# Performance work log

Hardware: AMD Instinct MI355X
Metric: run time of the kernel (lower is better)

## Reference

```python
import jax, jax.numpy as jnp
import numpy as np

N, NF, DIM, H, DH, DEPTH, EDIM, NB = 256, 127, 128, 8, 64, 6, 3, 512
INNER = H * DH  # 512
SCALE = DH ** -0.5
EPS = 1e-5


def setup_inputs() -> dict:
    key = jax.random.key(0)
    ks = jax.random.split(key, 16)
    p = lambda k, shape: jax.random.normal(k, shape, jnp.float32) * 0.02
    return {
        "coordinates": jax.random.normal(ks[0], (N, 3), jnp.float32),
        "bonds": jax.random.randint(ks[1], (NB, 2), 0, N),
        "noise_level": jax.random.uniform(ks[2], (1,), jnp.float32),
        "atom_emb": p(ks[3], (N, NF)),
        "ln1_g": jnp.ones((DEPTH, DIM)), "ln1_b": jnp.zeros((DEPTH, DIM)),
        "Wq": p(ks[4], (DEPTH, DIM, INNER)), "bq": jnp.zeros((DEPTH, INNER)),
        "Wkv": p(ks[5], (DEPTH, DIM, 2 * INNER)), "bkv": jnp.zeros((DEPTH, 2 * INNER)),
        "We": p(ks[6], (DEPTH, EDIM, INNER)), "be": jnp.zeros((DEPTH, INNER)),
        "Wo": p(ks[7], (DEPTH, INNER, DIM)), "bo": jnp.zeros((DEPTH, DIM)),
        "Wg1": p(ks[8], (DEPTH, 3 * DIM)),
        "ln2_g": jnp.ones((DEPTH, DIM)), "ln2_b": jnp.zeros((DEPTH, DIM)),
        "W1": p(ks[9], (DEPTH, DIM, 4 * DIM)), "b1": jnp.zeros((DEPTH, 4 * DIM)),
        "W2": p(ks[10], (DEPTH, 4 * DIM, DIM)), "b2": jnp.zeros((DEPTH, DIM)),
        "Wg2": p(ks[11], (DEPTH, 3 * DIM)),
        "out_w": p(ks[12], (DIM, 1)), "out_b": jnp.zeros((1,)),
    }


def _layernorm(x, g, b):
    m = jnp.mean(x, axis=-1, keepdims=True)
    v = jnp.mean((x - m) ** 2, axis=-1, keepdims=True)
    return (x - m) * jax.lax.rsqrt(v + EPS) * g + b


def _gated_residual(x, res, Wg):
    # Linear(3*dim -> 1, no bias) then sigmoid; mask is all-True so no masking.
    gate = jax.nn.sigmoid(jnp.concatenate([x, res, x - res], axis=-1) @ Wg)[..., None]
    return x * gate + res * (1.0 - gate)


def _forward(coordinates, bonds, noise_level, atom_emb, ln1_g, ln1_b, Wq, bq,
             Wkv, bkv, We, be, Wo, bo, Wg1, ln2_g, ln2_b, W1, b1, W2, b2, Wg2,
             out_w, out_b):
    n = coordinates.shape[0]
    # nodes: [n, NF] atom embeddings (looked up at arange(n)) + noise column -> [n, DIM]
    noise_col = jnp.broadcast_to(noise_level.reshape(1, 1), (n, 1))
    nodes = jnp.concatenate([atom_emb, noise_col], axis=-1)
    # dense edge tensor [n, n, 3]: coordinate differences at bonded pairs, antisymmetric
    bi, bj = bonds[:, 0], bonds[:, 1]
    diff = coordinates[bi] - coordinates[bj]
    edges = jnp.zeros((n, n, EDIM), jnp.float32).at[bi, bj].set(diff).at[bj, bi].set(-diff)

    for l in range(DEPTH):
        # --- edge-biased multi-head attention (PreNorm) ---
        x = _layernorm(nodes, ln1_g[l], ln1_b[l])
        q = (x @ Wq[l] + bq[l]).reshape(n, H, DH).transpose(1, 0, 2)          # [h, i, d]
        kv = x @ Wkv[l] + bkv[l]
        k = kv[:, :INNER].reshape(n, H, DH).transpose(1, 0, 2)                # [h, j, d]
        v = kv[:, INNER:].reshape(n, H, DH).transpose(1, 0, 2)                # [h, j, d]
        e = (edges @ We[l] + be[l]).reshape(n, n, H, DH).transpose(2, 0, 1, 3)  # [h, i, j, d]
        k_ij = k[:, None, :, :] + e                                            # [h, i, j, d]
        v_ij = v[:, None, :, :] + e
        sim = jnp.einsum('hid,hijd->hij', q, k_ij) * SCALE
        attn = jax.nn.softmax(sim, axis=-1)  # mask is all ones -> no-op
        out = jnp.einsum('hij,hijd->hid', attn, v_ij)                          # [h, i, d]
        out = out.transpose(1, 0, 2).reshape(n, INNER) @ Wo[l] + bo[l]         # [n, DIM]
        nodes = _gated_residual(out, nodes, Wg1[l])
        # --- feedforward (PreNorm) + gated residual ---
        y = _layernorm(nodes, ln2_g[l], ln2_b[l])
        y = jax.nn.gelu(y @ W1[l] + b1[l], approximate=False) @ W2[l] + b2[l]
        nodes = _gated_residual(y, nodes, Wg2[l])

    energy = nodes @ out_w + out_b  # [n, 1]
    return energy[None, :, :]       # [1, n, 1]


def reference(coordinates, bonds, noise_level, atom_emb, ln1_g, ln1_b, Wq, bq,
              Wkv, bkv, We, be, Wo, bo, Wg1, ln2_g, ln2_b, W1, b1, W2, b2, Wg2,
              out_w, out_b):
    return _forward(coordinates, bonds, noise_level, atom_emb, ln1_g, ln1_b,
                    Wq, bq, Wkv, bkv, We, be, Wo, bo, Wg1, ln2_g, ln2_b,
                    W1, b1, W2, b2, Wg2, out_w, out_b)
```

## Files before the change

### kernel.cpp

```cpp
#include <hip/hip_runtime.h>

#define NN     256
#define NF     127
#define DIM    128
#define NH     8
#define DH     64
#define INNER  512
#define DEPTH  6
#define NB     512
#define ATTN_SCALE 0.125f
#define LN_EPS 1e-5f

__device__ __forceinline__ float wred_sum(float v){
#pragma unroll
  for(int o=32;o;o>>=1) v += __shfl_xor(v,o);
  return v;
}
__device__ __forceinline__ float wred_max(float v){
#pragma unroll
  for(int o=32;o;o>>=1) v = fmaxf(v,__shfl_xor(v,o));
  return v;
}
__device__ __forceinline__ float block_sum(float v, float* sred, int t){
  v = wred_sum(v);
  __syncthreads();
  if((t&63)==0) sred[t>>6]=v;
  __syncthreads();
  float s = 0.f;
#pragma unroll
  for(int w=0; w<8; w++) s += sred[w];
  return s;
}

__device__ __forceinline__ void dev_ln(const float* in, float* out,
                                       const float* g, const float* b,
                                       float* sred, int t){
  float v = (t<DIM)? in[t] : 0.f;
  float m = block_sum(v,sred,t) * (1.f/DIM);
  float d = (t<DIM)? (v-m) : 0.f;
  float var = block_sum(d*d,sred,t) * (1.f/DIM);
  float rs = rsqrtf(var + LN_EPS);
  if(t<DIM) out[t] = d*rs*g[t] + b[t];
  __syncthreads();
}

__device__ __forceinline__ void dev_qkv4(const float* xs, int i,
    const float* Wq, const float* bq, const float* Wkv, const float* bkv,
    const float* be, float* qg, float* kT, float* vg, float* redS, int t){
  {
    const int cg4 = (t&127)*4, rq = t>>7;
    float4 acc = make_float4(0.f,0.f,0.f,0.f);
#pragma unroll
    for(int f=rq*32; f<rq*32+32; f++){
      float x = xs[f];
      float4 w = *(const float4*)(Wq + f*INNER + cg4);
      acc.x=fmaf(x,w.x,acc.x); acc.y=fmaf(x,w.y,acc.y);
      acc.z=fmaf(x,w.z,acc.z); acc.w=fmaf(x,w.w,acc.w);
    }
    *(float4*)(redS + rq*INNER + cg4) = acc;
  }
  __syncthreads();
  qg[i*INNER+t] = bq[t] + redS[t] + redS[INNER+t] + redS[2*INNER+t] + redS[3*INNER+t];
  __syncthreads();
  {
    const int cg4 = (t&255)*4, rh = t>>8;
    float4 acc = make_float4(0.f,0.f,0.f,0.f);
#pragma unroll 8
    for(int f=rh*64; f<rh*64+64; f++){
      float x = xs[f];
      float4 w = *(const float4*)(Wkv + f*(2*INNER) + cg4);
      acc.x=fmaf(x,w.x,acc.x); acc.y=fmaf(x,w.y,acc.y);
      acc.z=fmaf(x,w.z,acc.z); acc.w=fmaf(x,w.w,acc.w);
    }
    *(float4*)(redS + rh*(2*INNER) + cg4) = acc;
  }
  __syncthreads();
#pragma unroll
  for(int cc=0; cc<2; cc++){
    int c = t + cc*512;
    float s = redS[c] + redS[2*INNER+c] + bkv[c];
    if(c < INNER) kT[c*NN+i]          = s + be[c];
    else          vg[i*INNER+c-INNER] = s + be[c-INNER];
  }
  __syncthreads();
}

__global__ __launch_bounds__(512) void k_qkv0(const float* atom_emb, const float* noise,
    float* nodes,
    const float* ln1_g, const float* ln1_b,
    const float* Wq, const float* bq, const float* Wkv, const float* bkv, const float* be,
    float* qg, float* kT, float* vg){
  __shared__ float nd[DIM], xs[DIM], sred[8], redS[2048];
  int t = threadIdx.x, i = blockIdx.x;
  if(t<DIM){
    float v = (t<NF)? atom_emb[i*NF+t] : noise[0];
    nd[t] = v;
    nodes[i*DIM+t] = v;
  }
  __syncthreads();
  dev_ln(nd, xs, ln1_g, ln1_b, sred, t);
  dev_qkv4(xs, i, Wq, bq, Wkv, bkv, be, qg, kT, vg, redS, t);
}

__global__ __launch_bounds__(512) void k_layer(
    float* nodes, const float* qg, const float* kT, const float* vg,
    float* qg_n, float* kT_n, float* vg_n,
    const int* bonds, const float* coords,
    const float* We,
    const float* Wo, const float* bo, const float* Wg1,
    const float* ln2_g, const float* ln2_b,
    const float* W1, const float* b1, const float* W2, const float* b2,
    const float* Wg2,
    const float* ln1_g_n, const float* ln1_b_n,
    const float* Wq_n, const float* bq_n, const float* Wkv_n, const float* bkv_n,
    const float* be_n, int has_next)
{
  __shared__ float nd[DIM], xs[DIM], qs[INNER], ao[INNER], o128[DIM];
  __shared__ float eL[NN*3], aW[NH*NN], redS[2048], sred[8], qWe[NH*3];
  const int t = threadIdx.x, i = blockIdx.x;

  if(t<DIM) nd[t] = nodes[i*DIM+t];
  qs[t] = qg[i*INNER+t];
  eL[t] = 0.f;
  if(t<NN) eL[512+t] = 0.f;
  __syncthreads();

  {
    int bi = bonds[2*t], bj = bonds[2*t+1];
    if(bi==i || bj==i){
      float dx = coords[3*bi+0] - coords[3*bj+0];
      float dy = coords[3*bi+1] - coords[3*bj+1];
      float dz = coords[3*bi+2] - coords[3*bj+2];
      if(bi==i){ eL[bj*3+0]=dx;  eL[bj*3+1]=dy;  eL[bj*3+2]=dz;  }
      if(bj==i){ eL[bi*3+0]=-dx; eL[bi*3+1]=-dy; eL[bi*3+2]=-dz; }
    }
  }
  __syncthreads();

  if(t < NH*3){
    int h = t/3, c = t%3;
    float acc = 0.f;
    for(int d=0; d<DH; d++) acc = fmaf(qs[h*DH+d], We[c*INNER + h*DH + d], acc);
    qWe[t] = acc;
  }
  __syncthreads();

  {
    const int h = t>>6, l = t&63, j0 = 4*l;
    const float* kTh = kT + (h*DH)*NN;
    float s0=0.f,s1=0.f,s2=0.f,s3=0.f;
#pragma unroll 8
    for(int o=0; o<DH; o++){
      float qv = qs[h*DH+o];
      float4 kk = *(const float4*)(kTh + o*NN + j0);
      s0=fmaf(qv,kk.x,s0); s1=fmaf(qv,kk.y,s1); s2=fmaf(qv,kk.z,s2); s3=fmaf(qv,kk.w,s3);
    }
    float w0=qWe[h*3+0], w1=qWe[h*3+1], w2=qWe[h*3+2];
    s0 += w0*eL[(j0+0)*3+0] + w1*eL[(j0+0)*3+1] + w2*eL[(j0+0)*3+2];
    s1 += w0*eL[(j0+1)*3+0] + w1*eL[(j0+1)*3+1] + w2*eL[(j0+1)*3+2];
    s2 += w0*eL[(j0+2)*3+0] + w1*eL[(j0+2)*3+1] + w2*eL[(j0+2)*3+2];
    s3 += w0*eL[(j0+3)*3+0] + w1*eL[(j0+3)*3+1] + w2*eL[(j0+3)*3+2];
    s0*=ATTN_SCALE; s1*=ATTN_SCALE; s2*=ATTN_SCALE; s3*=ATTN_SCALE;
    float mx = wred_max(fmaxf(fmaxf(s0,s1),fmaxf(s2,s3)));
    float p0=expf(s0-mx), p1=expf(s1-mx), p2=expf(s2-mx), p3=expf(s3-mx);
    float inv = 1.f / wred_sum(p0+p1+p2+p3);
    float a0=p0*inv, a1=p1*inv, a2=p2*inv, a3=p3*inv;
    float* aw = aW + h*NN;
    *(float4*)(aw + j0) = make_float4(a0,a1,a2,a3);
    float c0 = a0*eL[(j0+0)*3+0]+a1*eL[(j0+1)*3+0]+a2*eL[(j0+2)*3+0]+a3*eL[(j0+3)*3+0];
    float c1 = a0*eL[(j0+0)*3+1]+a1*eL[(j0+1)*3+1]+a2*eL[(j0+2)*3+1]+a3*eL[(j0+3)*3+1];
    float c2 = a0*eL[(j0+0)*3+2]+a1*eL[(j0+1)*3+2]+a2*eL[(j0+2)*3+2]+a3*eL[(j0+3)*3+2];
    c0 = wred_sum(c0); c1 = wred_sum(c1); c2 = wred_sum(c2);
    __builtin_amdgcn_wave_barrier();
    const int dq = (l&15)*4, jg = l>>4;
    const float* vb = vg + h*DH + dq;
    float4 acc = make_float4(0.f,0.f,0.f,0.f);
#pragma unroll 8
    for(int jj=0; jj<64; jj++){
      int j = jg*64 + jj;
      float a = aw[j];
      float4 vv = *(const float4*)(vb + j*INNER);
      acc.x=fmaf(a,vv.x,acc.x); acc.y=fmaf(a,vv.y,acc.y);
      acc.z=fmaf(a,vv.z,acc.z); acc.w=fmaf(a,vv.w,acc.w);
    }
#pragma unroll
    for(int o=16;o<64;o<<=1){
      acc.x += __shfl_xor(acc.x,o); acc.y += __shfl_xor(acc.y,o);
      acc.z += __shfl_xor(acc.z,o); acc.w += __shfl_xor(acc.w,o);
    }
    if(l<16){
      float4 we0 = *(const float4*)(We + 0*INNER + h*DH + dq);
      float4 we1 = *(const float4*)(We + 1*INNER + h*DH + dq);
      float4 we2 = *(const float4*)(We + 2*INNER + h*DH + dq);
      float4 o;
      o.x = acc.x + c0*we0.x + c1*we1.x + c2*we2.x;
      o.y = acc.y + c0*we0.y + c1*we1.y + c2*we2.y;
      o.z = acc.z + c0*we0.z + c1*we1.z + c2*we2.z;
      o.w = acc.w + c0*we0.w + c1*we1.w + c2*we2.w;
      *(float4*)(ao + h*DH + dq) = o;
    }
  }
  __syncthreads();

  {
    const int cg4 = (t&31)*4, rg = t>>5;
    float4 acc = make_float4(0.f,0.f,0.f,0.f);
#pragma unroll
    for(int r=rg*32; r<rg*32+32; r++){
      float a = ao[r];
      float4 w = *(const float4*)(Wo + r*DIM + cg4);
      acc.x=fmaf(a,w.x,acc.x); acc.y=fmaf(a,w.y,acc.y);
      acc.z=fmaf(a,w.z,acc.z); acc.w=fmaf(a,w.w,acc.w);
    }
    *(float4*)(redS + rg*DIM + cg4) = acc;
    __syncthreads();
    if(t<DIM){
      float s = bo[t];
#pragma unroll
      for(int g=0; g<16; g++) s += redS[g*DIM+t];
      o128[t] = s;
    }
    __syncthreads();
    float gv = 0.f;
    if(t<DIM){
      float o = o128[t], r = nd[t];
      gv = o*Wg1[t] + r*Wg1[DIM+t] + (o-r)*Wg1[2*DIM+t];
    }
    float gs = block_sum(gv, sred, t);
    float gate = 1.f/(1.f + expf(-gs));
    if(t<DIM) nd[t] = o128[t]*gate + nd[t]*(1.f-gate);
    __syncthreads();
  }

  dev_ln(nd, xs, ln2_g, ln2_b, sred, t);
  {
    const int cg4 = (t&127)*4, rq = t>>7;
    float4 acc = make_float4(0.f,0.f,0.f,0.f);
#pragma unroll
    for(int f=rq*32; f<rq*32+32; f++){
      float x = xs[f];
      float4 w = *(const float4*)(W1 + f*INNER + cg4);
      acc.x=fmaf(x,w.x,acc.x); acc.y=fmaf(x,w.y,acc.y);
      acc.z=fmaf(x,w.z,acc.z); acc.w=fmaf(x,w.w,acc.w);
    }
    *(float4*)(redS + rq*INNER + cg4) = acc;
  }
  __syncthreads();
  {
    float a = b1[t] + redS[t] + redS[INNER+t] + redS[2*INNER+t] + redS[3*INNER+t];
    qs[t] = 0.5f*a*(1.f + erff(a*0.70710678118654752440f));
  }
  __syncthreads();
  {
    const int cg4 = (t&31)*4, rg = t>>5;
    float4 acc = make_float4(0.f,0.f,0.f,0.f);
#pragma unroll
    for(int m=rg*32; m<rg*32+32; m++){
      float a = qs[m];
      float4 w = *(const float4*)(W2 + m*DIM + cg4);
      acc.x=fmaf(a,w.x,acc.x); acc.y=fmaf(a,w.y,acc.y);
      acc.z=fmaf(a,w.z,acc.z); acc.w=fmaf(a,w.w,acc.w);
    }
    *(float4*)(redS + rg*DIM + cg4) = acc;
    __syncthreads();
    if(t<DIM){
      float s = b2[t];
#pragma unroll
      for(int g=0; g<16; g++) s += redS[g*DIM+t];
      o128[t] = s;
    }
    __syncthreads();
    float gv = 0.f;
    if(t<DIM){
      float y = o128[t], r = nd[t];
      gv = y*Wg2[t] + r*Wg2[DIM+t] + (y-r)*Wg2[2*DIM+t];
    }
    float gs = block_sum(gv, sred, t);
    float gate = 1.f/(1.f + expf(-gs));
    if(t<DIM) nd[t] = o128[t]*gate + nd[t]*(1.f-gate);
    __syncthreads();
  }
  if(t<DIM) nodes[i*DIM+t] = nd[t];

  if(has_next){
    dev_ln(nd, xs, ln1_g_n, ln1_b_n, sred, t);
    dev_qkv4(xs, i, Wq_n, bq_n, Wkv_n, bkv_n, be_n, qg_n, kT_n, vg_n, redS, t);
  }
}

__global__ __launch_bounds__(64) void k_energy(const float* nodes, const float* out_w,
                                               const float* out_b, float* out){
  int i = blockIdx.x, l = threadIdx.x;
  float a = fmaf(nodes[i*DIM+l], out_w[l], nodes[i*DIM+64+l]*out_w[64+l]);
  a = wred_sum(a);
  if(l==0) out[i] = a + out_b[0];
}

extern "C" void kernel_launch(void* const* d_in, const int* in_sizes, int n_in,
                              void* d_out, int out_size, void* d_ws, size_t ws_size,
                              hipStream_t stream){
  const float* coords   = (const float*)d_in[0];
  const int*   bonds    = (const int*  )d_in[1];
  const float* noise    = (const float*)d_in[2];
  const float* atom_emb = (const float*)d_in[3];
  const float* ln1_g = (const float*)d_in[4];
  const float* ln1_b = (const float*)d_in[5];
  const float* Wq    = (const float*)d_in[6];
  const float* bq    = (const float*)d_in[7];
  const float* Wkv   = (const float*)d_in[8];
  const float* bkv   = (const float*)d_in[9];
  const float* We    = (const float*)d_in[10];
  const float* be    = (const float*)d_in[11];
  const float* Wo    = (const float*)d_in[12];
  const float* bo    = (const float*)d_in[13];
  const float* Wg1   = (const float*)d_in[14];
  const float* ln2_g = (const float*)d_in[15];
  const float* ln2_b = (const float*)d_in[16];
  const float* W1    = (const float*)d_in[17];
  const float* b1    = (const float*)d_in[18];
  const float* W2    = (const float*)d_in[19];
  const float* b2    = (const float*)d_in[20];
  const float* Wg2   = (const float*)d_in[21];
  const float* out_w = (const float*)d_in[22];
  const float* out_b = (const float*)d_in[23];

  float* ws = (float*)d_ws;
  float* nodes   = ws;
  float* qbuf[2] = { ws +  32768, ws + 163840 };
  float* kbuf[2] = { ws + 294912, ws + 425984 };
  float* vbuf[2] = { ws + 557056, ws + 688128 };

  k_qkv0<<<256, 512, 0, stream>>>(atom_emb, noise, nodes, ln1_g, ln1_b,
                                  Wq, bq, Wkv, bkv, be,
                                  qbuf[0], kbuf[0], vbuf[0]);
  for(int l=0; l<DEPTH; l++){
    int cur = l&1, nxt = cur^1;
    int has_next = (l < DEPTH-1);
    int ln = has_next ? l+1 : l;
    k_layer<<<256, 512, 0, stream>>>(
      nodes, qbuf[cur], kbuf[cur], vbuf[cur],
      qbuf[nxt], kbuf[nxt], vbuf[nxt],
      bonds, coords,
      We  + (size_t)l*3*INNER,
      Wo  + (size_t)l*INNER*DIM, bo + (size_t)l*DIM, Wg1 + (size_t)l*3*DIM,
      ln2_g + (size_t)l*DIM, ln2_b + (size_t)l*DIM,
      W1  + (size_t)l*DIM*4*DIM, b1 + (size_t)l*4*DIM,
      W2  + (size_t)l*4*DIM*DIM, b2 + (size_t)l*DIM, Wg2 + (size_t)l*3*DIM,
      ln1_g + (size_t)ln*DIM, ln1_b + (size_t)ln*DIM,
      Wq  + (size_t)ln*DIM*INNER, bq + (size_t)ln*INNER,
      Wkv + (size_t)ln*DIM*2*INNER, bkv + (size_t)ln*2*INNER,
      be  + (size_t)ln*INNER, has_next);
  }
  k_energy<<<256, 64, 0, stream>>>(nodes, out_w, out_b, (float*)d_out);
}
```

Measured before the change: 320.2 us.

## Process four atoms per block to reuse weight and K/V loads

Each block now handles four node rows instead of one, so every weight, K and V element loaded from global memory feeds four rows of FMAs. Grid size drops from 256 to 64 blocks. The final energy projection is folded into the last layer kernel, which removes a separate launch. The cost is fewer blocks than compute units on the GPU, plus more registers and shared memory per block, which lowers parallelism and occupancy.

After: 510.9 us. 59.5% more time.

```diff
diff --git a/kernel.cpp b/kernel.cpp
--- a/kernel.cpp
+++ b/kernel.cpp
@@ -8,98 +8,153 @@
 #define INNER  512
 #define DEPTH  6
 #define NB     512
+#define R      4
 #define ATTN_SCALE 0.125f
 #define LN_EPS 1e-5f
 
+#define FMA4(A_, S_, V_) { A_.x=fmaf(S_,(V_).x,A_.x); A_.y=fmaf(S_,(V_).y,A_.y); \
+                           A_.z=fmaf(S_,(V_).z,A_.z); A_.w=fmaf(S_,(V_).w,A_.w); }
+
 __device__ __forceinline__ float wred_sum(float v){
 #pragma unroll
   for(int o=32;o;o>>=1) v += __shfl_xor(v,o);
   return v;
 }
-__device__ __forceinline__ float wred_max(float v){
-#pragma unroll
-  for(int o=32;o;o>>=1) v = fmaxf(v,__shfl_xor(v,o));
-  return v;
-}
-__device__ __forceinline__ float block_sum(float v, float* sred, int t){
+
+__device__ __forceinline__ float row_sum128(float v, float* sred, int t){
   v = wred_sum(v);
   __syncthreads();
-  if((t&63)==0) sred[t>>6]=v;
-  __syncthreads();
-  float s = 0.f;
-#pragma unroll
-  for(int w=0; w<8; w++) s += sred[w];
-  return s;
-}
-
-__device__ __forceinline__ void dev_ln(const float* in, float* out,
-                                       const float* g, const float* b,
-                                       float* sred, int t){
-  float v = (t<DIM)? in[t] : 0.f;
-  float m = block_sum(v,sred,t) * (1.f/DIM);
-  float d = (t<DIM)? (v-m) : 0.f;
-  float var = block_sum(d*d,sred,t) * (1.f/DIM);
-  float rs = rsqrtf(var + LN_EPS);
-  if(t<DIM) out[t] = d*rs*g[t] + b[t];
-  __syncthreads();
-}
-
-__device__ __forceinline__ void dev_qkv4(const float* xs, int i,
+  if((t&63)==0) sred[t>>6] = v;
+  __syncthreads();
+  const int r2 = (t>>7)<<1;
+  return sred[r2] + sred[r2+1];
+}
+
+__device__ __forceinline__ void dev_ln4(const float* in, float* out,
+                                        const float* g, const float* b,
+                                        float* sred, int t){
+  const int d = t&127;
+  float v = in[t];
+  float m = row_sum128(v, sred, t) * (1.f/DIM);
+  float dv = v - m;
+  float var = row_sum128(dv*dv, sred, t) * (1.f/DIM);
+  out[t] = dv * rsqrtf(var + LN_EPS) * g[d] + b[d];
+  __syncthreads();
+}
+
+__device__ __forceinline__ void dev_gate(const float* o, float* nd, const float* Wg,
+                                         float* sred, int t){
+  const int d = t&127;
+  float ov = o[t], rv = nd[t];
+  float gv = ov*Wg[d] + rv*Wg[DIM+d] + (ov-rv)*Wg[2*DIM+d];
+  float gate = 1.f/(1.f + expf(-row_sum128(gv, sred, t)));
+  nd[t] = ov*gate + rv*(1.f-gate);
+  __syncthreads();
+}
+
+__device__ __forceinline__ void mm128_512_part(const float* xin, const float* W,
+                                               float* SC, int t){
+  const int cg4 = (t&127)<<2, fq = t>>7;
+  float4 a0=make_float4(0.f,0.f,0.f,0.f), a1=a0, a2=a0, a3=a0;
+#pragma unroll 8
+  for(int f=fq*32; f<fq*32+32; f++){
+    float4 wv = *(const float4*)(W + f*INNER + cg4);
+    float v0=xin[f], v1=xin[DIM+f], v2=xin[2*DIM+f], v3=xin[3*DIM+f];
+    FMA4(a0,v0,wv); FMA4(a1,v1,wv); FMA4(a2,v2,wv); FMA4(a3,v3,wv);
+  }
+  float* p = SC + (fq*R)*INNER + cg4;
+  *(float4*)(p)           = a0;
+  *(float4*)(p +   INNER) = a1;
+  *(float4*)(p + 2*INNER) = a2;
+  *(float4*)(p + 3*INNER) = a3;
+}
+
+__device__ __forceinline__ void mm128_1024_part(const float* xin, const float* W,
+                                                float* SC, int t){
+  const int cg4 = (t&255)<<2, fh = t>>8;
+  float4 a0=make_float4(0.f,0.f,0.f,0.f), a1=a0, a2=a0, a3=a0;
+#pragma unroll 8
+  for(int f=fh*64; f<fh*64+64; f++){
+    float4 wv = *(const float4*)(W + f*(2*INNER) + cg4);
+    float v0=xin[f], v1=xin[DIM+f], v2=xin[2*DIM+f], v3=xin[3*DIM+f];
+    FMA4(a0,v0,wv); FMA4(a1,v1,wv); FMA4(a2,v2,wv); FMA4(a3,v3,wv);
+  }
+  float* p = SC + (fh*R)*(2*INNER) + cg4;
+  *(float4*)(p)             = a0;
+  *(float4*)(p +   2*INNER) = a1;
+  *(float4*)(p + 2*2*INNER) = a2;
+  *(float4*)(p + 3*2*INNER) = a3;
+}
+
+__device__ __forceinline__ void mm512_128_part(const float* ain, const float* W,
+                                               float* SC, int t){
+  const int cg4 = (t&31)<<2, fg = t>>5;
+  float4 a0=make_float4(0.f,0.f,0.f,0.f), a1=a0, a2=a0, a3=a0;
+#pragma unroll 8
+  for(int f=fg*32; f<fg*32+32; f++){
+    float4 wv = *(const float4*)(W + f*DIM + cg4);
+    float v0=ain[f], v1=ain[INNER+f], v2=ain[2*INNER+f], v3=ain[3*INNER+f];
+    FMA4(a0,v0,wv); FMA4(a1,v1,wv); FMA4(a2,v2,wv); FMA4(a3,v3,wv);
+  }
+  float* p = SC + (fg*R)*DIM + cg4;
+  *(float4*)(p)         = a0;
+  *(float4*)(p +   DIM) = a1;
+  *(float4*)(p + 2*DIM) = a2;
+  *(float4*)(p + 3*DIM) = a3;
+}
+
+__device__ __forceinline__ void red512_128(const float* SC, const float* bias,
+                                           float* o128, int t){
+  const int r = t>>7, d = t&127;
+  float s = bias[d];
+#pragma unroll
+  for(int fg=0; fg<16; fg++) s += SC[(fg*R + r)*DIM + d];
+  o128[t] = s;
+}
+
+__device__ __forceinline__ void dev_qkv(const float* xs, int i0,
     const float* Wq, const float* bq, const float* Wkv, const float* bkv,
-    const float* be, float* qg, float* kT, float* vg, float* redS, int t){
-  {
-    const int cg4 = (t&127)*4, rq = t>>7;
-    float4 acc = make_float4(0.f,0.f,0.f,0.f);
-#pragma unroll
-    for(int f=rq*32; f<rq*32+32; f++){
-      float x = xs[f];
-      float4 w = *(const float4*)(Wq + f*INNER + cg4);
-      acc.x=fmaf(x,w.x,acc.x); acc.y=fmaf(x,w.y,acc.y);
-      acc.z=fmaf(x,w.z,acc.z); acc.w=fmaf(x,w.w,acc.w);
-    }
-    *(float4*)(redS + rq*INNER + cg4) = acc;
-  }
-  __syncthreads();
-  qg[i*INNER+t] = bq[t] + redS[t] + redS[INNER+t] + redS[2*INNER+t] + redS[3*INNER+t];
-  __syncthreads();
-  {
-    const int cg4 = (t&255)*4, rh = t>>8;
-    float4 acc = make_float4(0.f,0.f,0.f,0.f);
-#pragma unroll 8
-    for(int f=rh*64; f<rh*64+64; f++){
-      float x = xs[f];
-      float4 w = *(const float4*)(Wkv + f*(2*INNER) + cg4);
-      acc.x=fmaf(x,w.x,acc.x); acc.y=fmaf(x,w.y,acc.y);
-      acc.z=fmaf(x,w.z,acc.z); acc.w=fmaf(x,w.w,acc.w);
-    }
-    *(float4*)(redS + rh*(2*INNER) + cg4) = acc;
-  }
-  __syncthreads();
-#pragma unroll
-  for(int cc=0; cc<2; cc++){
-    int c = t + cc*512;
-    float s = redS[c] + redS[2*INNER+c] + bkv[c];
-    if(c < INNER) kT[c*NN+i]          = s + be[c];
-    else          vg[i*INNER+c-INNER] = s + be[c-INNER];
+    const float* be, float* qg, float* kT, float* vg, float* SC, int t){
+  mm128_512_part(xs, Wq, SC, t);
+  __syncthreads();
+#pragma unroll
+  for(int cc=0; cc<4; cc++){
+    int idx = cc*512 + t;
+    int r = idx>>9, c = idx&511;
+    float s = bq[c] + SC[r*INNER+c] + SC[(R+r)*INNER+c]
+                    + SC[(2*R+r)*INNER+c] + SC[(3*R+r)*INNER+c];
+    qg[(i0+r)*INNER + c] = s;
+  }
+  __syncthreads();
+  mm128_1024_part(xs, Wkv, SC, t);
+  __syncthreads();
+#pragma unroll
+  for(int cc=0; cc<8; cc++){
+    int idx = cc*512 + t;
+    int r = idx>>10, c = idx&1023;
+    float s = bkv[c] + SC[r*(2*INNER)+c] + SC[(R+r)*(2*INNER)+c];
+    if(c < INNER) kT[c*NN + i0 + r]            = s + be[c];
+    else          vg[(i0+r)*INNER + (c-INNER)] = s + be[c-INNER];
   }
   __syncthreads();
 }
 
 __global__ __launch_bounds__(512) void k_qkv0(const float* atom_emb, const float* noise,
-    float* nodes,
-    const float* ln1_g, const float* ln1_b,
+    float* nodes, const float* ln1_g, const float* ln1_b,
     const float* Wq, const float* bq, const float* Wkv, const float* bkv, const float* be,
     float* qg, float* kT, float* vg){
-  __shared__ float nd[DIM], xs[DIM], sred[8], redS[2048];
-  int t = threadIdx.x, i = blockIdx.x;
-  if(t<DIM){
-    float v = (t<NF)? atom_emb[i*NF+t] : noise[0];
+  __shared__ __align__(16) float SC[8192];
+  __shared__ float nd[R*DIM], xsm[R*DIM], sred[8];
+  const int t = threadIdx.x, i0 = blockIdx.x*R;
+  {
+    const int r = t>>7, d = t&127;
+    float v = (d<NF)? atom_emb[(i0+r)*NF + d] : noise[0];
     nd[t] = v;
-    nodes[i*DIM+t] = v;
-  }
-  __syncthreads();
-  dev_ln(nd, xs, ln1_g, ln1_b, sred, t);
-  dev_qkv4(xs, i, Wq, bq, Wkv, bkv, be, qg, kT, vg, redS, t);
+    nodes[i0*DIM + t] = v;
+  }
+  __syncthreads();
+  dev_ln4(nd, xsm, ln1_g, ln1_b, sred, t);
+  dev_qkv(xsm, i0, Wq, bq, Wkv, bkv, be, qg, kT, vg, SC, t);
 }
 
 __global__ __launch_bounds__(512) void k_layer(
@@ -113,187 +168,213 @@
     const float* Wg2,
     const float* ln1_g_n, const float* ln1_b_n,
     const float* Wq_n, const float* bq_n, const float* Wkv_n, const float* bkv_n,
-    const float* be_n, int has_next)
+    const float* be_n,
+    const float* out_w, const float* out_b, float* eout, int has_next)
 {
-  __shared__ float nd[DIM], xs[DIM], qs[INNER], ao[INNER], o128[DIM];
-  __shared__ float eL[NN*3], aW[NH*NN], redS[2048], sred[8], qWe[NH*3];
-  const int t = threadIdx.x, i = blockIdx.x;
-
-  if(t<DIM) nd[t] = nodes[i*DIM+t];
-  qs[t] = qg[i*INNER+t];
-  eL[t] = 0.f;
-  if(t<NN) eL[512+t] = 0.f;
+  __shared__ __align__(16) float SC[8192];
+  __shared__ __align__(16) float qs[R*INNER];
+  __shared__ __align__(16) float eb[3*R*NN];
+  __shared__ __align__(16) float ao[R*INNER];
+  __shared__ float nd[R*DIM], xsm[R*DIM];
+  float* o128 = eb;
+  float* sred = eb + R*DIM;
+  const int t = threadIdx.x, i0 = blockIdx.x*R;
+
+  nd[t] = nodes[i0*DIM + t];
+#pragma unroll
+  for(int cc=0; cc<4; cc++) qs[cc*512 + t] = qg[i0*INNER + cc*512 + t];
+#pragma unroll
+  for(int cc=0; cc<6; cc++) eb[cc*512 + t] = 0.f;
   __syncthreads();
 
   {
-    int bi = bonds[2*t], bj = bonds[2*t+1];
-    if(bi==i || bj==i){
+    const int bi = bonds[2*t], bj = bonds[2*t+1];
+    const bool hi = (bi>=i0 && bi<i0+R), hj = (bj>=i0 && bj<i0+R);
+    if(hi || hj){
       float dx = coords[3*bi+0] - coords[3*bj+0];
       float dy = coords[3*bi+1] - coords[3*bj+1];
       float dz = coords[3*bi+2] - coords[3*bj+2];
-      if(bi==i){ eL[bj*3+0]=dx;  eL[bj*3+1]=dy;  eL[bj*3+2]=dz;  }
-      if(bj==i){ eL[bi*3+0]=-dx; eL[bi*3+1]=-dy; eL[bi*3+2]=-dz; }
-    }
-  }
-  __syncthreads();
-
-  if(t < NH*3){
-    int h = t/3, c = t%3;
-    float acc = 0.f;
-    for(int d=0; d<DH; d++) acc = fmaf(qs[h*DH+d], We[c*INNER + h*DH + d], acc);
-    qWe[t] = acc;
+      if(hi){ int r = bi-i0;
+        eb[r*NN+bj]=dx;  eb[(R+r)*NN+bj]=dy;  eb[(2*R+r)*NN+bj]=dz;  }
+      if(hj){ int r = bj-i0;
+        eb[r*NN+bi]=-dx; eb[(R+r)*NN+bi]=-dy; eb[(2*R+r)*NN+bi]=-dz; }
+    }
   }
   __syncthreads();
 
   {
-    const int h = t>>6, l = t&63, j0 = 4*l;
-    const float* kTh = kT + (h*DH)*NN;
-    float s0=0.f,s1=0.f,s2=0.f,s3=0.f;
+    const int h = t>>6, l = t&63, j0 = l<<2;
+    const int qb = h*DH;
+    float qwe[R][3];
+    {
+      float qv0=qs[0*INNER+qb+l], qv1=qs[1*INNER+qb+l],
+            qv2=qs[2*INNER+qb+l], qv3=qs[3*INNER+qb+l];
+#pragma unroll
+      for(int c=0;c<3;c++){
+        float wv = We[c*INNER + qb + l];
+        qwe[0][c]=qv0*wv; qwe[1][c]=qv1*wv; qwe[2][c]=qv2*wv; qwe[3][c]=qv3*wv;
+      }
+#pragma unroll
+      for(int o=32;o;o>>=1)
+#pragma unroll
+        for(int r=0;r<R;r++){
+          qwe[r][0]+=__shfl_xor(qwe[r][0],o);
+          qwe[r][1]+=__shfl_xor(qwe[r][1],o);
+          qwe[r][2]+=__shfl_xor(qwe[r][2],o);
+        }
+    }
+    const float* kTh = kT + qb*NN;
+    float s[R][4];
+#pragma unroll
+    for(int r=0;r<R;r++){ s[r][0]=0.f; s[r][1]=0.f; s[r][2]=0.f; s[r][3]=0.f; }
 #pragma unroll 8
-    for(int o=0; o<DH; o++){
-      float qv = qs[h*DH+o];
+    for(int o=0;o<DH;o++){
       float4 kk = *(const float4*)(kTh + o*NN + j0);
-      s0=fmaf(qv,kk.x,s0); s1=fmaf(qv,kk.y,s1); s2=fmaf(qv,kk.z,s2); s3=fmaf(qv,kk.w,s3);
-    }
-    float w0=qWe[h*3+0], w1=qWe[h*3+1], w2=qWe[h*3+2];
-    s0 += w0*eL[(j0+0)*3+0] + w1*eL[(j0+0)*3+1] + w2*eL[(j0+0)*3+2];
-    s1 += w0*eL[(j0+1)*3+0] + w1*eL[(j0+1)*3+1] + w2*eL[(j0+1)*3+2];
-    s2 += w0*eL[(j0+2)*3+0] + w1*eL[(j0+2)*3+1] + w2*eL[(j0+2)*3+2];
-    s3 += w0*eL[(j0+3)*3+0] + w1*eL[(j0+3)*3+1] + w2*eL[(j0+3)*3+2];
-    s0*=ATTN_SCALE; s1*=ATTN_SCALE; s2*=ATTN_SCALE; s3*=ATTN_SCALE;
-    float mx = wred_max(fmaxf(fmaxf(s0,s1),fmaxf(s2,s3)));
-    float p0=expf(s0-mx), p1=expf(s1-mx), p2=expf(s2-mx), p3=expf(s3-mx);
-    float inv = 1.f / wred_sum(p0+p1+p2+p3);
-    float a0=p0*inv, a1=p1*inv, a2=p2*inv, a3=p3*inv;
-    float* aw = aW + h*NN;
-    *(float4*)(aw + j0) = make_float4(a0,a1,a2,a3);
-    float c0 = a0*eL[(j0+0)*3+0]+a1*eL[(j0+1)*3+0]+a2*eL[(j0+2)*3+0]+a3*eL[(j0+3)*3+0];
-    float c1 = a0*eL[(j0+0)*3+1]+a1*eL[(j0+1)*3+1]+a2*eL[(j0+2)*3+1]+a3*eL[(j0+3)*3+1];
-    float c2 = a0*eL[(j0+0)*3+2]+a1*eL[(j0+1)*3+2]+a2*eL[(j0+2)*3+2]+a3*eL[(j0+3)*3+2];
-    c0 = wred_sum(c0); c1 = wred_sum(c1); c2 = wred_sum(c2);
+#pragma unroll
+      for(int r=0;r<R;r++){
+        float qv = qs[r*INNER + qb + o];
+        s[r][0]=fmaf(qv,kk.x,s[r][0]); s[r][1]=fmaf(qv,kk.y,s[r][1]);
+        s[r][2]=fmaf(qv,kk.z,s[r][2]); s[r][3]=fmaf(qv,kk.w,s[r][3]);
+      }
+    }
+#pragma unroll
+    for(int r=0;r<R;r++){
+      float4 ex = *(const float4*)(eb + r*NN + j0);
+      float4 ey = *(const float4*)(eb + (R+r)*NN + j0);
+      float4 ez = *(const float4*)(eb + (2*R+r)*NN + j0);
+      float w0=qwe[r][0], w1=qwe[r][1], w2=qwe[r][2];
+      s[r][0] = (s[r][0] + w0*ex.x + w1*ey.x + w2*ez.x)*ATTN_SCALE;
+      s[r][1] = (s[r][1] + w0*ex.y + w1*ey.y + w2*ez.y)*ATTN_SCALE;
+      s[r][2] = (s[r][2] + w0*ex.z + w1*ey.z + w2*ez.z)*ATTN_SCALE;
+      s[r][3] = (s[r][3] + w0*ex.w + w1*ey.w + w2*ez.w)*ATTN_SCALE;
+    }
+    float mx[R];
+#pragma unroll
+    for(int r=0;r<R;r++) mx[r]=fmaxf(fmaxf(s[r][0],s[r][1]),fmaxf(s[r][2],s[r][3]));
+#pragma unroll
+    for(int o=32;o;o>>=1)
+#pragma unroll
+      for(int r=0;r<R;r++) mx[r]=fmaxf(mx[r],__shfl_xor(mx[r],o));
+    float sm[R];
+#pragma unroll
+    for(int r=0;r<R;r++){
+      s[r][0]=expf(s[r][0]-mx[r]); s[r][1]=expf(s[r][1]-mx[r]);
+      s[r][2]=expf(s[r][2]-mx[r]); s[r][3]=expf(s[r][3]-mx[r]);
+      sm[r]=s[r][0]+s[r][1]+s[r][2]+s[r][3];
+    }
+#pragma unroll
+    for(int o=32;o;o>>=1)
+#pragma unroll
+      for(int r=0;r<R;r++) sm[r]+=__shfl_xor(sm[r],o);
+    float cE[R][3];
+#pragma unroll
+    for(int r=0;r<R;r++){
+      float inv = 1.f/sm[r];
+      float a0=s[r][0]*inv, a1=s[r][1]*inv, a2=s[r][2]*inv, a3=s[r][3]*inv;
+      *(float4*)(SC + ((r<<3)+h)*NN + j0) = make_float4(a0,a1,a2,a3);
+      float4 ex = *(const float4*)(eb + r*NN + j0);
+      float4 ey = *(const float4*)(eb + (R+r)*NN + j0);
+      float4 ez = *(const float4*)(eb + (2*R+r)*NN + j0);
+      cE[r][0]=a0*ex.x+a1*ex.y+a2*ex.z+a3*ex.w;
+      cE[r][1]=a0*ey.x+a1*ey.y+a2*ey.z+a3*ey.w;
+      cE[r][2]=a0*ez.x+a1*ez.y+a2*ez.z+a3*ez.w;
+    }
+#pragma unroll
+    for(int o=32;o;o>>=1)
+#pragma unroll
+      for(int r=0;r<R;r++){
+        cE[r][0]+=__shfl_xor(cE[r][0],o);
+        cE[r][1]+=__shfl_xor(cE[r][1],o);
+        cE[r][2]+=__shfl_xor(cE[r][2],o);
+      }
     __builtin_amdgcn_wave_barrier();
-    const int dq = (l&15)*4, jg = l>>4;
-    const float* vb = vg + h*DH + dq;
-    float4 acc = make_float4(0.f,0.f,0.f,0.f);
+    const int dq=(l&15)<<2, jg=l>>4;
+    const float* vb = vg + qb + dq;
+    float4 acc0=make_float4(0.f,0.f,0.f,0.f), acc1=acc0, acc2=acc0, acc3=acc0;
 #pragma unroll 8
-    for(int jj=0; jj<64; jj++){
-      int j = jg*64 + jj;
-      float a = aw[j];
+    for(int jj=0;jj<64;jj++){
+      int j = (jg<<6) + ((jj + (jg<<3)) & 63);
       float4 vv = *(const float4*)(vb + j*INNER);
-      acc.x=fmaf(a,vv.x,acc.x); acc.y=fmaf(a,vv.y,acc.y);
-      acc.z=fmaf(a,vv.z,acc.z); acc.w=fmaf(a,vv.w,acc.w);
+      float w0 = SC[(0*NH+h)*NN + j];
+      float w1 = SC[(1*NH+h)*NN + j];
+      float w2 = SC[(2*NH+h)*NN + j];
+      float w3 = SC[(3*NH+h)*NN + j];
+      FMA4(acc0,w0,vv); FMA4(acc1,w1,vv); FMA4(acc2,w2,vv); FMA4(acc3,w3,vv);
     }
 #pragma unroll
     for(int o=16;o<64;o<<=1){
-      acc.x += __shfl_xor(acc.x,o); acc.y += __shfl_xor(acc.y,o);
-      acc.z += __shfl_xor(acc.z,o); acc.w += __shfl_xor(acc.w,o);
+      acc0.x+=__shfl_xor(acc0.x,o); acc0.y+=__shfl_xor(acc0.y,o);
+      acc0.z+=__shfl_xor(acc0.z,o); acc0.w+=__shfl_xor(acc0.w,o);
+      acc1.x+=__shfl_xor(acc1.x,o); acc1.y+=__shfl_xor(acc1.y,o);
+      acc1.z+=__shfl_xor(acc1.z,o); acc1.w+=__shfl_xor(acc1.w,o);
+      acc2.x+=__shfl_xor(acc2.x,o); acc2.y+=__shfl_xor(acc2.y,o);
+      acc2.z+=__shfl_xor(acc2.z,o); acc2.w+=__shfl_xor(acc2.w,o);
+      acc3.x+=__shfl_xor(acc3.x,o); acc3.y+=__shfl_xor(acc3.y,o);
+      acc3.z+=__shfl_xor(acc3.z,o); acc3.w+=__shfl_xor(acc3.w,o);
     }
     if(l<16){
-      float4 we0 = *(const float4*)(We + 0*INNER + h*DH + dq);
-      float4 we1 = *(const float4*)(We + 1*INNER + h*DH + dq);
-      float4 we2 = *(const float4*)(We + 2*INNER + h*DH + dq);
-      float4 o;
-      o.x = acc.x + c0*we0.x + c1*we1.x + c2*we2.x;
-      o.y = acc.y + c0*we0.y + c1*we1.y + c2*we2.y;
-      o.z = acc.z + c0*we0.z + c1*we1.z + c2*we2.z;
-      o.w = acc.w + c0*we0.w + c1*we1.w + c2*we2.w;
-      *(float4*)(ao + h*DH + dq) = o;
-    }
-  }
-  __syncthreads();
-
-  {
-    const int cg4 = (t&31)*4, rg = t>>5;
-    float4 acc = make_float4(0.f,0.f,0.f,0.f);
-#pragma unroll
-    for(int r=rg*32; r<rg*32+32; r++){
-      float a = ao[r];
-      float4 w = *(const float4*)(Wo + r*DIM + cg4);
-      acc.x=fmaf(a,w.x,acc.x); acc.y=fmaf(a,w.y,acc.y);
-      acc.z=fmaf(a,w.z,acc.z); acc.w=fmaf(a,w.w,acc.w);
-    }
-    *(float4*)(redS + rg*DIM + cg4) = acc;
-    __syncthreads();
-    if(t<DIM){
-      float s = bo[t];
-#pragma unroll
-      for(int g=0; g<16; g++) s += redS[g*DIM+t];
-      o128[t] = s;
-    }
-    __syncthreads();
-    float gv = 0.f;
-    if(t<DIM){
-      float o = o128[t], r = nd[t];
-      gv = o*Wg1[t] + r*Wg1[DIM+t] + (o-r)*Wg1[2*DIM+t];
-    }
-    float gs = block_sum(gv, sred, t);
-    float gate = 1.f/(1.f + expf(-gs));
-    if(t<DIM) nd[t] = o128[t]*gate + nd[t]*(1.f-gate);
-    __syncthreads();
-  }
-
-  dev_ln(nd, xs, ln2_g, ln2_b, sred, t);
-  {
-    const int cg4 = (t&127)*4, rq = t>>7;
-    float4 acc = make_float4(0.f,0.f,0.f,0.f);
-#pragma unroll
-    for(int f=rq*32; f<rq*32+32; f++){
-      float x = xs[f];
-      float4 w = *(const float4*)(W1 + f*INNER + cg4);
-      acc.x=fmaf(x,w.x,acc.x); acc.y=fmaf(x,w.y,acc.y);
-      acc.z=fmaf(x,w.z,acc.z); acc.w=fmaf(x,w.w,acc.w);
-    }
-    *(float4*)(redS + rq*INNER + cg4) = acc;
-  }
-  __syncthreads();
-  {
-    float a = b1[t] + redS[t] + redS[INNER+t] + redS[2*INNER+t] + redS[3*INNER+t];
-    qs[t] = 0.5f*a*(1.f + erff(a*0.70710678118654752440f));
-  }
-  __syncthreads();
-  {
-    const int cg4 = (t&31)*4, rg = t>>5;
-    float4 acc = make_float4(0.f,0.f,0.f,0.f);
-#pragma unroll
-    for(int m=rg*32; m<rg*32+32; m++){
-      float a = qs[m];
-      float4 w = *(const float4*)(W2 + m*DIM + cg4);
-      acc.x=fmaf(a,w.x,acc.x); acc.y=fmaf(a,w.y,acc.y);
-      acc.z=fmaf(a,w.z,acc.z); acc.w=fmaf(a,w.w,acc.w);
-    }
-    *(float4*)(redS + rg*DIM + cg4) = acc;
-    __syncthreads();
-    if(t<DIM){
-      float s = b2[t];
-#pragma unroll
-      for(int g=0; g<16; g++) s += redS[g*DIM+t];
-      o128[t] = s;
-    }
-    __syncthreads();
-    float gv = 0.f;
-    if(t<DIM){
-      float y = o128[t], r = nd[t];
-      gv = y*Wg2[t] + r*Wg2[DIM+t] + (y-r)*Wg2[2*DIM+t];
-    }
-    float gs = block_sum(gv, sred, t);
-    float gate = 1.f/(1.f + expf(-gs));
-    if(t<DIM) nd[t] = o128[t]*gate + nd[t]*(1.f-gate);
-    __syncthreads();
-  }
-  if(t<DIM) nodes[i*DIM+t] = nd[t];
+      float4 we0 = *(const float4*)(We + 0*INNER + qb + dq);
+      float4 we1 = *(const float4*)(We + 1*INNER + qb + dq);
+      float4 we2 = *(const float4*)(We + 2*INNER + qb + dq);
+      float4 ov;
+      ov.x=acc0.x+cE[0][0]*we0.x+cE[0][1]*we1.x+cE[0][2]*we2.x;
+      ov.y=acc0.y+cE[0][0]*we0.y+cE[0][1]*we1.y+cE[0][2]*we2.y;
+      ov.z=acc0.z+cE[0][0]*we0.z+cE[0][1]*we1.z+cE[0][2]*we2.z;
+      ov.w=acc0.w+cE[0][0]*we0.w+cE[0][1]*we1.w+cE[0][2]*we2.w;
+      *(float4*)(ao + 0*INNER + qb + dq) = ov;
+      ov.x=acc1.x+cE[1][0]*we0.x+cE[1][1]*we1.x+cE[1][2]*we2.x;
+      ov.y=acc1.y+cE[1][0]*we0.y+cE[1][1]*we1.y+cE[1][2]*we2.y;
+      ov.z=acc1.z+cE[1][0]*we0.z+cE[1][1]*we1.z+cE[1][2]*we2.z;
+      ov.w=acc1.w+cE[1][0]*we0.w+cE[1][1]*we1.w+cE[1][2]*we2.w;
+      *(float4*)(ao + 1*INNER + qb + dq) = ov;
+      ov.x=acc2.x+cE[2][0]*we0.x+cE[2][1]*we1.x+cE[2][2]*we2.x;
+      ov.y=acc2.y+cE[2][0]*we0.y+cE[2][1]*we1.y+cE[2][2]*we2.y;
+      ov.z=acc2.z+cE[2][0]*we0.z+cE[2][1]*we1.z+cE[2][2]*we2.z;
+      ov.w=acc2.w+cE[2][0]*we0.w+cE[2][1]*we1.w+cE[2][2]*we2.w;
+      *(float4*)(ao + 2*INNER + qb + dq) = ov;
+      ov.x=acc3.x+cE[3][0]*we0.x+cE[3][1]*we1.x+cE[3][2]*we2.x;
+      ov.y=acc3.y+cE[3][0]*we0.y+cE[3][1]*we1.y+cE[3][2]*we2.y;
+      ov.z=acc3.z+cE[3][0]*we0.z+cE[3][1]*we1.z+cE[3][2]*we2.z;
+      ov.w=acc3.w+cE[3][0]*we0.w+cE[3][1]*we1.w+cE[3][2]*we2.w;
+      *(float4*)(ao + 3*INNER + qb + dq) = ov;
+    }
+  }
+  __syncthreads();
+
+  mm512_128_part(ao, Wo, SC, t);
+  __syncthreads();
+  red512_128(SC, bo, o128, t);
+  __syncthreads();
+  dev_gate(o128, nd, Wg1, sred, t);
+
+  dev_ln4(nd, xsm, ln2_g, ln2_b, sred, t);
+  mm128_512_part(xsm, W1, SC, t);
+  __syncthreads();
+#pragma unroll
+  for(int cc=0; cc<4; cc++){
+    int idx = cc*512 + t;
+    int r = idx>>9, c = idx&511;
+    float a = b1[c] + SC[r*INNER+c] + SC[(R+r)*INNER+c]
+                    + SC[(2*R+r)*INNER+c] + SC[(3*R+r)*INNER+c];
+    qs[idx] = 0.5f*a*(1.f + erff(a*0.70710678118654752440f));
+  }
+  __syncthreads();
+  mm512_128_part(qs, W2, SC, t);
+  __syncthreads();
+  red512_128(SC, b2, o128, t);
+  __syncthreads();
+  dev_gate(o128, nd, Wg2, sred, t);
+
+  nodes[i0*DIM + t] = nd[t];
 
   if(has_next){
-    dev_ln(nd, xs, ln1_g_n, ln1_b_n, sred, t);
-    dev_qkv4(xs, i, Wq_n, bq_n, Wkv_n, bkv_n, be_n, qg_n, kT_n, vg_n, redS, t);
-  }
-}
-
-__global__ __launch_bounds__(64) void k_energy(const float* nodes, const float* out_w,
-                                               const float* out_b, float* out){
-  int i = blockIdx.x, l = threadIdx.x;
-  float a = fmaf(nodes[i*DIM+l], out_w[l], nodes[i*DIM+64+l]*out_w[64+l]);
-  a = wred_sum(a);
-  if(l==0) out[i] = a + out_b[0];
+    dev_ln4(nd, xsm, ln1_g_n, ln1_b_n, sred, t);
+    dev_qkv(xsm, i0, Wq_n, bq_n, Wkv_n, bkv_n, be_n, qg_n, kT_n, vg_n, SC, t);
+  } else {
+    float ev = nd[t] * out_w[t&127];
+    float es = row_sum128(ev, sred, t);
+    if((t&127)==0) eout[i0 + (t>>7)] = es + out_b[0];
+  }
 }
 
 extern "C" void kernel_launch(void* const* d_in, const int* in_sizes, int n_in,
@@ -330,14 +411,14 @@
   float* kbuf[2] = { ws + 294912, ws + 425984 };
   float* vbuf[2] = { ws + 557056, ws + 688128 };
 
-  k_qkv0<<<256, 512, 0, stream>>>(atom_emb, noise, nodes, ln1_g, ln1_b,
-                                  Wq, bq, Wkv, bkv, be,
-                                  qbuf[0], kbuf[0], vbuf[0]);
+  k_qkv0<<<NN/R, 512, 0, stream>>>(atom_emb, noise, nodes, ln1_g, ln1_b,
+                                   Wq, bq, Wkv, bkv, be,
+                                   qbuf[0], kbuf[0], vbuf[0]);
   for(int l=0; l<DEPTH; l++){
     int cur = l&1, nxt = cur^1;
     int has_next = (l < DEPTH-1);
     int ln = has_next ? l+1 : l;
-    k_layer<<<256, 512, 0, stream>>>(
+    k_layer<<<NN/R, 512, 0, stream>>>(
       nodes, qbuf[cur], kbuf[cur], vbuf[cur],
       qbuf[nxt], kbuf[nxt], vbuf[nxt],
       bonds, coords,
@@ -349,7 +430,7 @@
       ln1_g + (size_t)ln*DIM, ln1_b + (size_t)ln*DIM,
       Wq  + (size_t)ln*DIM*INNER, bq + (size_t)ln*INNER,
       Wkv + (size_t)ln*DIM*2*INNER, bkv + (size_t)ln*2*INNER,
-      be  + (size_t)ln*INNER, has_next);
-  }
-  k_energy<<<256, 64, 0, stream>>>(nodes, out_w, out_b, (float*)d_out);
-}
+      be  + (size_t)ln*INNER,
+      out_w, out_b, (float*)d_out, has_next);
+  }
+}
```
